# Kernel optimization log

Measured on AMD Instinct MI355X. Metric: run time of the kernel, lower is better.

## Reference

```python
import jax, jax.numpy as jnp
import numpy as np

LMAX = 8                         # lmax-1 used by s2/so3 irreps
DIMS = [2 * l + 1 for l in range(LMAX + 1)]
S2_OFF = np.cumsum([0] + DIMS).tolist()            # offsets into 81-dim s2 irreps
SO3_OFF = np.cumsum([0] + [d * d for d in DIMS]).tolist()  # offsets into 969-dim so3 irreps
S2_DIM = S2_OFF[-1]              # 81
SO3_DIM = SO3_OFF[-1]            # 969
F_IN = 81                        # multiplicity into S2Conv
F_SO3 = 300
C = 768                          # encoder feature channels
KS = 7                           # encoder feature map / kernel size
B = 8
G_S2 = 48                        # s2 healpix grid rec_level=1
G_ACT = 4096                     # SO3Activation grid points (stand-in for res=20 grid)
G_SO3 = 36864                    # so3 healpix grid rec_level=3


def setup_inputs() -> dict:
    key = jax.random.key(0)
    ks = jax.random.split(key, 7)
    return {
        "x": jax.random.normal(ks[0], (B, C, KS, KS), jnp.float32),
        "F": jax.random.normal(ks[1], (F_IN, S2_DIM * C, KS, KS), jnp.float32) * 0.02,
        "w_s2": jax.random.normal(ks[2], (F_IN, F_SO3, G_S2), jnp.float32) * 0.1,
        "Y": jax.random.normal(ks[3], (G_S2, S2_DIM), jnp.float32),
        "w_so3": jax.random.normal(ks[4], (F_SO3, 1, G_SO3), jnp.float32) * 0.1,
        "D": jax.random.normal(ks[5], (G_SO3, SO3_DIM), jnp.float32),
        "D_act": jax.random.normal(ks[6], (G_ACT, SO3_DIM), jnp.float32),
    }


def _forward(x, F, w_s2, Y, w_so3, D, D_act):
    b = x.shape[0]
    # ---- Induction layer: split expanded R2Conv filter into 768-channel chunks,
    # stack, contract with feature map. g_split: (n=81, c_out=81, C, 7, 7)
    g = jnp.swapaxes(F.reshape(F_IN, S2_DIM, C, KS, KS), 0, 1)
    y = jnp.einsum('ijkhw,akhw->aji', g, x)          # (B, 81, 81): (batch, f_in, s2 irreps)

    # ---- S2Conv: expand kernel into irrep space, per-l block linear (s2 -> so3 irreps)
    psi = jnp.einsum('ni,xyn->xyi', Y, w_s2) / np.sqrt(G_S2)  # (81, 300, 81)
    outs = []
    for l, d in enumerate(DIMS):
        o = S2_OFF[l]
        xl = y[:, :, o:o + d]                        # (B, f_in, 2l+1)
        wl = psi[:, :, o:o + d]                      # (f_in, f_out, mul_out=2l+1)
        ol = jnp.einsum('bfm,fgu->bgum', xl, wl) / np.sqrt(F_IN)
        outs.append(ol.reshape(b, F_SO3, d * d))
    z = jnp.concatenate(outs, axis=-1)               # (B, 300, 969)

    # ---- SO3Activation: to grid, relu, back to irreps
    s = jnp.einsum('bfi,gi->bfg', z, D_act)
    z = jnp.einsum('bfg,gi->bfi', jax.nn.relu(s), D_act) / G_ACT

    # ---- SO3Conv: expand kernel via Wigner-D buffer, per-l block linear (so3 -> so3)
    psi2 = jnp.einsum('ni,xyn->xyi', D, w_so3) / np.sqrt(G_SO3)  # (300, 1, 969)
    outs = []
    for l, d in enumerate(DIMS):
        o = SO3_OFF[l]
        xl = z[:, :, o:o + d * d].reshape(b, F_SO3, d, d)   # (B, f, u, m)
        wl = psi2[:, :, o:o + d * d].reshape(F_SO3, 1, d, d)  # (f, g, v, u)
        ol = jnp.einsum('bfum,fgvu->bgvm', xl, wl) / np.sqrt(F_SO3 * d)
        outs.append(ol.reshape(b, 1, d * d))
    return jnp.concatenate(outs, axis=-1)            # (B, 1, 969)


def reference(x, F, w_s2, Y, w_so3, D, D_act):
    return _forward(x, F, w_s2, Y, w_so3, D, D_act)
```

## Files before the change

kernel.cpp:

```cpp
#include <hip/hip_runtime.h>
#include <hip/hip_bf16.h>
#include <math.h>

#define THREADS 256

constexpr int B_    = 8;
constexpr int C_    = 768;
constexpr int KS_   = 7;
constexpr int F_IN  = 81;
constexpr int F_SO3 = 300;
constexpr int S2_DIM  = 81;
constexpr int SO3_DIM = 969;
constexpr int G_S2  = 48;
constexpr int G_ACT = 4096;
constexpr int G_SO3 = 36864;
constexpr int CKK   = C_ * KS_ * KS_;
constexpr int CKK4  = CKK / 4;
constexpr int NPAIR = F_IN * S2_DIM;

constexpr int D2_SPLIT = 4;
constexpr int E1_SPLIT = 32;
constexpr int F_SPLIT  = 5;

__constant__ int d_S2_OFF[10]  = {0, 1, 4, 9, 16, 25, 36, 49, 64, 81};
__constant__ int d_SO3_OFF[10] = {0, 1, 10, 35, 84, 165, 286, 455, 680, 969};

using short8 = __attribute__((ext_vector_type(8))) short;
using f32x4  = __attribute__((ext_vector_type(4))) float;

#define GL16(gp, lp)                                                        \
  __builtin_amdgcn_global_load_lds(                                         \
      (const __attribute__((address_space(1))) void*)(gp),                  \
      (__attribute__((address_space(3))) void*)(lp), 16, 0, 0)

constexpr size_t AL(size_t x) { return (x + 1023) & ~(size_t)1023; }
constexpr size_t O_Y     = 0;
constexpr size_t O_PSI   = O_Y     + AL((size_t)8 * NPAIR * 4);
constexpr size_t O_ZBF   = O_PSI   + AL((size_t)F_IN * F_SO3 * 81 * 4);
constexpr size_t O_DACT  = O_ZBF   + AL((size_t)2432 * 1024 * 2);
constexpr size_t O_DACTT = O_DACT  + AL((size_t)4096 * 1024 * 2);
constexpr size_t O_WSO3  = O_DACTT + AL((size_t)1024 * 4096 * 2);
constexpr size_t O_DT    = O_WSO3  + AL((size_t)384 * 36864 * 2);
constexpr size_t O_SBF   = O_DT    + AL((size_t)1024 * 36864 * 2);
constexpr size_t O_D2P   = O_SBF   + AL((size_t)2432 * 4096 * 2);
constexpr size_t O_Z2P   = O_D2P   + AL((size_t)D2_SPLIT * 2432 * 1024 * 4);
constexpr size_t O_E1P   = O_Z2P   + AL((size_t)2432 * 1024 * 4);
constexpr size_t O_PSI2  = O_E1P   + AL((size_t)E1_SPLIT * 384 * 1024 * 4);
constexpr size_t O_SFP   = O_PSI2  + AL((size_t)F_SO3 * SO3_DIM * 4);
constexpr size_t FAST_NEED = O_SFP + AL((size_t)F_SPLIT * 8 * SO3_DIM * 4);

constexpr size_t WS_Y    = 0;
constexpr size_t WS_PSI  = 52488;
constexpr size_t WS_Z    = 2020788;
constexpr size_t WS_S    = 4346388;
constexpr size_t WS_Z2   = 14176788;
constexpr size_t WS_P2P  = 16502388;
constexpr size_t WS_PSI2 = 18827988;

__global__ __launch_bounds__(THREADS) void k_stage_a3(
    const float* __restrict__ Fm, const float* __restrict__ x, float* __restrict__ y) {
  const int p0  = blockIdx.x * 3;
  const int tid = threadIdx.x;
  const float4* __restrict__ F4 = (const float4*)Fm;
  const float4* __restrict__ x4 = (const float4*)x;

  float acc[3][8];
#pragma unroll
  for (int p = 0; p < 3; ++p)
#pragma unroll
    for (int b = 0; b < 8; ++b) acc[p][b] = 0.f;

  for (int i = tid; i < CKK4; i += THREADS) {
    float4 xv[8];
#pragma unroll
    for (int b = 0; b < 8; ++b) xv[b] = x4[b * CKK4 + i];
#pragma unroll
    for (int p = 0; p < 3; ++p) {
      float4 fv = F4[(size_t)(p0 + p) * CKK4 + i];
#pragma unroll
      for (int b = 0; b < 8; ++b)
        acc[p][b] += fv.x * xv[b].x + fv.y * xv[b].y + fv.z * xv[b].z + fv.w * xv[b].w;
    }
  }

  __shared__ float red[4][24];
  const int lane = tid & 63, wid = tid >> 6;
#pragma unroll
  for (int p = 0; p < 3; ++p) {
#pragma unroll
    for (int b = 0; b < 8; ++b) {
      float v = acc[p][b];
      v += __shfl_down(v, 32);
      v += __shfl_down(v, 16);
      v += __shfl_down(v, 8);
      v += __shfl_down(v, 4);
      v += __shfl_down(v, 2);
      v += __shfl_down(v, 1);
      if (lane == 0) red[wid][p * 8 + b] = v;
    }
  }
  __syncthreads();
  if (tid < 24) {
    float v = red[0][tid] + red[1][tid] + red[2][tid] + red[3][tid];
    int p = tid / 8, b = tid % 8;
    y[(size_t)b * NPAIR + p0 + p] = v;
  }
}

__global__ __launch_bounds__(THREADS) void k_psi(
    const float* __restrict__ w_s2, const float* __restrict__ Y, float* __restrict__ psi) {
  int idx = blockIdx.x * THREADS + threadIdx.x;
  if (idx >= F_IN * F_SO3 * S2_DIM) return;
  int s  = idx % S2_DIM;
  int fg = idx / S2_DIM;
  const float* w = w_s2 + (size_t)fg * G_S2;
  float acc = 0.f;
#pragma unroll 8
  for (int n = 0; n < G_S2; ++n) acc += w[n] * Y[n * S2_DIM + s];
  psi[idx] = acc * 0.14433756729740643f;
}

__global__ __launch_bounds__(THREADS) void k_stage_c_bf(
    const float* __restrict__ y, const float* __restrict__ psi, __hip_bfloat16* __restrict__ z) {
  const int b = blockIdx.x / F_SO3;
  const int g = blockIdx.x % F_SO3;
  __shared__ float ybl[NPAIR];
  __shared__ float psl[NPAIR];
  const int tid = threadIdx.x;
  for (int t = tid; t < NPAIR; t += THREADS) {
    ybl[t] = y[(size_t)b * NPAIR + t];
    int f = t / S2_DIM, s = t % S2_DIM;
    psl[t] = psi[((size_t)f * F_SO3 + g) * S2_DIM + s];
  }
  __syncthreads();
  for (int i = tid; i < 1024; i += THREADS) {
    float acc = 0.f;
    if (i < SO3_DIM) {
      int l = 0;
      while (i >= d_SO3_OFF[l + 1]) ++l;
      int d  = 2 * l + 1;
      int r  = i - d_SO3_OFF[l];
      int u  = r / d, m = r - u * d;
      int so = d_S2_OFF[l];
#pragma unroll 9
      for (int f = 0; f < F_IN; ++f)
        acc += ybl[f * S2_DIM + so + m] * psl[f * S2_DIM + so + u];
      acc *= (1.0f / 9.0f);
    }
    z[((size_t)b * F_SO3 + g) * 1024 + i] = __float2bfloat16(acc);
  }
}

__global__ __launch_bounds__(THREADS) void k_stage_c(
    const float* __restrict__ y, const float* __restrict__ psi, float* __restrict__ z) {
  const int b = blockIdx.x / F_SO3;
  const int g = blockIdx.x % F_SO3;
  __shared__ float ybl[NPAIR];
  __shared__ float psl[NPAIR];
  const int tid = threadIdx.x;
  for (int t = tid; t < NPAIR; t += THREADS) {
    ybl[t] = y[(size_t)b * NPAIR + t];
    int f = t / S2_DIM, s = t % S2_DIM;
    psl[t] = psi[((size_t)f * F_SO3 + g) * S2_DIM + s];
  }
  __syncthreads();
  for (int i = tid; i < SO3_DIM; i += THREADS) {
    int l = 0;
    while (i >= d_SO3_OFF[l + 1]) ++l;
    int d  = 2 * l + 1;
    int r  = i - d_SO3_OFF[l];
    int u  = r / d, m = r - u * d;
    int so = d_S2_OFF[l];
    float acc = 0.f;
#pragma unroll 9
    for (int f = 0; f < F_IN; ++f)
      acc += ybl[f * S2_DIM + so + m] * psl[f * S2_DIM + so + u];
    z[((size_t)b * F_SO3 + g) * SO3_DIM + i] = acc * (1.0f / 9.0f);
  }
}

__global__ __launch_bounds__(THREADS) void k_cvt_pad(
    const float* __restrict__ src, __hip_bfloat16* __restrict__ dst,
    int R, int Cs, int Cp, int Rp) {
  size_t idx = (size_t)blockIdx.x * THREADS + threadIdx.x;
  size_t total = (size_t)Rp * Cp;
  if (idx >= total) return;
  int r = (int)(idx / Cp), c = (int)(idx % Cp);
  float v = (r < R && c < Cs) ? src[(size_t)r * Cs + c] : 0.f;
  dst[idx] = __float2bfloat16(v);
}

__global__ __launch_bounds__(THREADS) void k_transpose_cvt(
    const float* __restrict__ src, __hip_bfloat16* __restrict__ dst,
    int R, int Cs, size_t dstStride) {
  __shared__ float tile[32][33];
  const int c0 = blockIdx.x * 32, r0 = blockIdx.y * 32;
  const int tx = threadIdx.x & 31, ty = threadIdx.x >> 5;
#pragma unroll
  for (int i = 0; i < 32; i += 8) {
    int r = r0 + ty + i, c = c0 + tx;
    tile[ty + i][tx] = (r < R && c < Cs) ? src[(size_t)r * Cs + c] : 0.f;
  }
  __syncthreads();
#pragma unroll
  for (int i = 0; i < 32; i += 8) {
    int c = c0 + ty + i, r = r0 + tx;
    if (c < Cs && r < R) dst[(size_t)c * dstStride + r] = __float2bfloat16(tile[tx][ty + i]);
  }
}

template <int EPI>
__global__ __launch_bounds__(THREADS) void k_mfma_nt(
    const __hip_bfloat16* __restrict__ A, const __hip_bfloat16* __restrict__ B,
    void* __restrict__ Cout, int K, int kSpan, int Ncols, float scale, size_t splitStride) {
  __shared__ __align__(16) char smem[32768];
  char* As = smem;
  char* Bs = smem + 16384;

  const int gx = gridDim.x, gy = gridDim.y;
  unsigned nwg = (unsigned)gx * gy * gridDim.z;
  unsigned lin = ((unsigned)blockIdx.z * gy + blockIdx.y) * gx + blockIdx.x;
  if ((nwg & 7u) == 0u) {
    unsigned q = nwg >> 3;
    lin = (lin & 7u) * q + (lin >> 3);
  }
  const int bxi = (int)(lin % (unsigned)gx);
  const unsigned t1 = lin / (unsigned)gx;
  const int byi = (int)(t1 % (unsigned)gy);
  const int bzi = (int)(t1 / (unsigned)gy);

  const int t    = threadIdx.x;
  const int lane = t & 63;
  const int wave = t >> 6;
  const int wr   = wave >> 1, wc = wave & 1;
  const int bm = byi * 128, bn = bxi * 128;
  const int kBegin = bzi * kSpan;
  const int kEnd   = kBegin + kSpan;

  const char* pA[4];
  const char* pB[4];
  int ldsOff[4];
#pragma unroll
  for (int i = 0; i < 4; ++i) {
    int L   = i * 4096 + t * 16;
    int row = L >> 7;
    int kb  = (L & 127) ^ ((row & 7) << 4);
    pA[i] = (const char*)A + ((size_t)(bm + row) * K) * 2 + kb;
    pB[i] = (const char*)B + ((size_t)(bn + row) * K) * 2 + kb;
    ldsOff[i] = L;
  }

  f32x4 acc[4][4] = {};

  for (int k0 = kBegin; k0 < kEnd; k0 += 64) {
    size_t koff = (size_t)k0 * 2;
#pragma unroll
    for (int i = 0; i < 4; ++i) {
      GL16(pA[i] + koff, As + ldsOff[i]);
      GL16(pB[i] + koff, Bs + ldsOff[i]);
    }
    __syncthreads();
#pragma unroll
    for (int kk = 0; kk < 2; ++kk) {
      const int klin = kk * 64 + ((lane >> 4) << 4);
      short8 af[4], bfr[4];
#pragma unroll
      for (int m = 0; m < 4; ++m) {
        int ra = (wr << 6) + (m << 4) + (lane & 15);
        af[m] = *(const short8*)(As + ra * 128 + (klin ^ ((ra & 7) << 4)));
        int rb = (wc << 6) + (m << 4) + (lane & 15);
        bfr[m] = *(const short8*)(Bs + rb * 128 + (klin ^ ((rb & 7) << 4)));
      }
#pragma unroll
      for (int m = 0; m < 4; ++m)
#pragma unroll
        for (int n = 0; n < 4; ++n)
          acc[m][n] = __builtin_amdgcn_mfma_f32_16x16x32_bf16(af[m], bfr[n], acc[m][n], 0, 0, 0);
    }
    __syncthreads();
  }

  const int rbase = bm + (wr << 6) + ((lane >> 4) << 2);
  const int cbase = bn + (wc << 6) + (lane & 15);
  if (EPI == 0) {
    float* C = (float*)Cout + (size_t)bzi * splitStride;
#pragma unroll
    for (int m = 0; m < 4; ++m)
#pragma unroll
      for (int n = 0; n < 4; ++n)
#pragma unroll
        for (int r = 0; r < 4; ++r)
          C[(size_t)(rbase + m * 16 + r) * Ncols + (cbase + n * 16)] = acc[m][n][r] * scale;
  } else {
    __hip_bfloat16* C = (__hip_bfloat16*)Cout;
#pragma unroll
    for (int m = 0; m < 4; ++m)
#pragma unroll
      for (int n = 0; n < 4; ++n)
#pragma unroll
        for (int r = 0; r < 4; ++r)
          C[(size_t)(rbase + m * 16 + r) * Ncols + (cbase + n * 16)] =
              __float2bfloat16(fmaxf(acc[m][n][r], 0.f));
  }
}

__global__ __launch_bounds__(THREADS) void k_reduce_split(
    const float* __restrict__ parts, float* __restrict__ dst, int R, int C,
    size_t rowStride, size_t splitStride, size_t dstStride, int nSplit, float scale) {
  int idx = blockIdx.x * THREADS + threadIdx.x;
  if (idx >= R * C) return;
  int r = idx / C, c = idx % C;
  float a = 0.f;
  for (int s = 0; s < nSplit; ++s) a += parts[(size_t)s * splitStride + (size_t)r * rowStride + c];
  dst[(size_t)r * dstStride + c] = a * scale;
}

__global__ __launch_bounds__(THREADS) void k_stage_f_part(
    const float* __restrict__ z2, const float* __restrict__ psi2, float* __restrict__ partial,
    int zStride) {
  const int b  = blockIdx.x / 9;
  const int l  = blockIdx.x % 9;
  const int sp = blockIdx.y;
  const int d = 2 * l + 1, d2 = d * d;
  const int off = d_SO3_OFF[l];
  __shared__ float zb[10][289];
  __shared__ float pb[10][289];
  const int tid = threadIdx.x;
  float acc[2] = {0.f, 0.f};
  const int fBeg = sp * (F_SO3 / F_SPLIT), fEnd = fBeg + F_SO3 / F_SPLIT;
  for (int fc = fBeg; fc < fEnd; fc += 10) {
    for (int t = tid; t < 10 * d2; t += THREADS) {
      int fl = t / d2, q = t - fl * d2;
      int f  = fc + fl;
      zb[fl][q] = z2[((size_t)b * F_SO3 + f) * zStride + off + q];
      pb[fl][q] = psi2[(size_t)f * SO3_DIM + off + q];
    }
    __syncthreads();
#pragma unroll 2
    for (int io = 0; io < 2; ++io) {
      int i = tid + io * THREADS;
      if (i < d2) {
        int v = i / d, m = i - v * d;
        float a = acc[io];
#pragma unroll
        for (int fl = 0; fl < 10; ++fl) {
          float s_ = 0.f;
          for (int u = 0; u < d; ++u)
            s_ += zb[fl][u * d + m] * pb[fl][v * d + u];
          a += s_;
        }
        acc[io] = a;
      }
    }
    __syncthreads();
  }
  for (int io = 0; io < 2; ++io) {
    int i = tid + io * THREADS;
    if (i < d2) partial[((size_t)sp * 8 + b) * SO3_DIM + off + i] = acc[io];
  }
}

__global__ __launch_bounds__(THREADS) void k_stage_f_red(
    const float* __restrict__ partial, float* __restrict__ out) {
  int idx = blockIdx.x * THREADS + threadIdx.x;
  if (idx >= 8 * SO3_DIM) return;
  int b = idx / SO3_DIM, i = idx % SO3_DIM;
  int l = 0;
  while (i >= d_SO3_OFF[l + 1]) ++l;
  float a = 0.f;
#pragma unroll
  for (int sp = 0; sp < F_SPLIT; ++sp)
    a += partial[((size_t)sp * 8 + b) * SO3_DIM + i];
  out[(size_t)b * SO3_DIM + i] = a * rsqrtf(300.0f * (float)(2 * l + 1));
}

__global__ __launch_bounds__(THREADS) void k_gemm_nt_relu(
    const float* __restrict__ A, const float* __restrict__ Bm, float* __restrict__ Cm,
    int M, int N, int K) {
  __shared__ float As[16][68];
  __shared__ float Bs[16][68];
  const int bm = blockIdx.y * 64, bn = blockIdx.x * 64;
  const int t  = threadIdx.x;
  const int lk = t & 15, lm = t >> 4;
  const int tn = t & 15, tm = t >> 4;
  float acc[4][4] = {};
  for (int k0 = 0; k0 < K; k0 += 16) {
    int gk = k0 + lk;
#pragma unroll
    for (int j = 0; j < 4; ++j) {
      int m  = lm + 16 * j;
      int gm = bm + m;
      As[lk][m] = (gm < M && gk < K) ? A[(size_t)gm * K + gk] : 0.f;
      int gn = bn + m;
      Bs[lk][m] = (gn < N && gk < K) ? Bm[(size_t)gn * K + gk] : 0.f;
    }
    __syncthreads();
#pragma unroll
    for (int k = 0; k < 16; ++k) {
      float4 av = *(const float4*)&As[k][tm * 4];
      float4 bv = *(const float4*)&Bs[k][tn * 4];
      float a[4] = {av.x, av.y, av.z, av.w};
      float bb[4] = {bv.x, bv.y, bv.z, bv.w};
#pragma unroll
      for (int i2 = 0; i2 < 4; ++i2)
#pragma unroll
        for (int j2 = 0; j2 < 4; ++j2)
          acc[i2][j2] += a[i2] * bb[j2];
    }
    __syncthreads();
  }
#pragma unroll
  for (int i2 = 0; i2 < 4; ++i2) {
    int gm = bm + tm * 4 + i2;
    if (gm >= M) continue;
#pragma unroll
    for (int j2 = 0; j2 < 4; ++j2) {
      int gn = bn + tn * 4 + j2;
      if (gn < N) Cm[(size_t)gm * N + gn] = fmaxf(acc[i2][j2], 0.f);
    }
  }
}

__global__ __launch_bounds__(THREADS) void k_gemm_nn(
    const float* __restrict__ A, const float* __restrict__ Bm, float* __restrict__ Cm,
    int M, int N, int K, int kSpan, float scale, size_t cStride) {
  __shared__ float As[16][68];
  __shared__ float Bs[16][68];
  const int bm = blockIdx.y * 64, bn = blockIdx.x * 64;
  const int t   = threadIdx.x;
  const int lk  = t & 15, lm = t >> 4;
  const int ln  = t & 63, lkq = t >> 6;
  const int tn  = t & 15, tm = t >> 4;
  const int kBegin = blockIdx.z * kSpan;
  const int kEnd   = kBegin + kSpan;
  float* C = Cm + (size_t)blockIdx.z * cStride;
  float acc[4][4] = {};
  for (int k0 = kBegin; k0 < kEnd; k0 += 16) {
    {
      int gk = k0 + lk;
#pragma unroll
      for (int j = 0; j < 4; ++j) {
        int m = lm + 16 * j, gm = bm + m;
        As[lk][m] = (gm < M) ? A[(size_t)gm * K + gk] : 0.f;
      }
    }
    {
      int gn = bn + ln;
#pragma unroll
      for (int j = 0; j < 4; ++j) {
        int k = lkq + 4 * j;
        Bs[k][ln] = (gn < N) ? Bm[(size_t)(k0 + k) * N + gn] : 0.f;
      }
    }
    __syncthreads();
#pragma unroll
    for (int k = 0; k < 16; ++k) {
      float4 av = *(const float4*)&As[k][tm * 4];
      float4 bv = *(const float4*)&Bs[k][tn * 4];
      float a[4] = {av.x, av.y, av.z, av.w};
      float bb[4] = {bv.x, bv.y, bv.z, bv.w};
#pragma unroll
      for (int i2 = 0; i2 < 4; ++i2)
#pragma unroll
        for (int j2 = 0; j2 < 4; ++j2)
          acc[i2][j2] += a[i2] * bb[j2];
    }
    __syncthreads();
  }
#pragma unroll
  for (int i2 = 0; i2 < 4; ++i2) {
    int gm = bm + tm * 4 + i2;
    if (gm >= M) continue;
#pragma unroll
    for (int j2 = 0; j2 < 4; ++j2) {
      int gn = bn + tn * 4 + j2;
      if (gn < N) C[(size_t)gm * N + gn] = acc[i2][j2] * scale;
    }
  }
}

__global__ __launch_bounds__(THREADS) void k_reduce_psi2(
    const float* __restrict__ parts, float* __restrict__ psi2) {
  int idx = blockIdx.x * THREADS + threadIdx.x;
  if (idx >= F_SO3 * SO3_DIM) return;
  float acc = 0.f;
#pragma unroll
  for (int s = 0; s < 8; ++s) acc += parts[(size_t)s * (F_SO3 * SO3_DIM) + idx];
  psi2[idx] = acc * (1.0f / 192.0f);
}

__global__ __launch_bounds__(THREADS) void k_stage_f(
    const float* __restrict__ z2, const float* __restrict__ psi2, float* __restrict__ out,
    int zStride) {
  const int b = blockIdx.x / 9;
  const int l = blockIdx.x % 9;
  const int d = 2 * l + 1, d2 = d * d;
  const int off = d_SO3_OFF[l];
  __shared__ float zb[10][289];
  __shared__ float pb[10][289];
  const int tid = threadIdx.x;
  float acc[2] = {0.f, 0.f};
  const float scale = rsqrtf(300.0f * (float)d);
  for (int fc = 0; fc < F_SO3; fc += 10) {
    for (int t = tid; t < 10 * d2; t += THREADS) {
      int fl = t / d2, q = t - fl * d2;
      int f  = fc + fl;
      zb[fl][q] = z2[((size_t)b * F_SO3 + f) * zStride + off + q];
      pb[fl][q] = psi2[(size_t)f * SO3_DIM + off + q];
    }
    __syncthreads();
#pragma unroll 2
    for (int io = 0; io < 2; ++io) {
      int i = tid + io * THREADS;
      if (i < d2) {
        int v = i / d, m = i - v * d;
        float a = acc[io];
#pragma unroll
        for (int fl = 0; fl < 10; ++fl) {
          float s_ = 0.f;
          for (int u = 0; u < d; ++u)
            s_ += zb[fl][u * d + m] * pb[fl][v * d + u];
          a += s_;
        }
        acc[io] = a;
      }
    }
    __syncthreads();
  }
  for (int io = 0; io < 2; ++io) {
    int i = tid + io * THREADS;
    if (i < d2) out[(size_t)b * SO3_DIM + off + i] = acc[io] * scale;
  }
}

extern "C" void kernel_launch(void* const* d_in, const int* in_sizes, int n_in,
                              void* d_out, int out_size, void* d_ws, size_t ws_size,
                              hipStream_t stream) {
  const float* x     = (const float*)d_in[0];
  const float* Fm    = (const float*)d_in[1];
  const float* w_s2  = (const float*)d_in[2];
  const float* Y     = (const float*)d_in[3];
  const float* w_so3 = (const float*)d_in[4];
  const float* D     = (const float*)d_in[5];
  const float* D_act = (const float*)d_in[6];
  float* out = (float*)d_out;

  if (ws_size >= FAST_NEED) {
    char* p = (char*)d_ws;
    float*          y       = (float*)(p + O_Y);
    float*          psi     = (float*)(p + O_PSI);
    __hip_bfloat16* z_bf    = (__hip_bfloat16*)(p + O_ZBF);
    __hip_bfloat16* Dact_bf = (__hip_bfloat16*)(p + O_DACT);
    __hip_bfloat16* DactT_bf= (__hip_bfloat16*)(p + O_DACTT);
    __hip_bfloat16* wso3_bf = (__hip_bfloat16*)(p + O_WSO3);
    __hip_bfloat16* DT_bf   = (__hip_bfloat16*)(p + O_DT);
    __hip_bfloat16* s_bf    = (__hip_bfloat16*)(p + O_SBF);
    float*          d2p     = (float*)(p + O_D2P);
    float*          z2p     = (float*)(p + O_Z2P);
    float*          e1p     = (float*)(p + O_E1P);
    float*          psi2    = (float*)(p + O_PSI2);
    float*          sfp     = (float*)(p + O_SFP);

    k_cvt_pad<<<(4096 * 1024 + THREADS - 1) / THREADS, THREADS, 0, stream>>>(
        D_act, Dact_bf, G_ACT, SO3_DIM, 1024, 4096);
    k_transpose_cvt<<<dim3(31, 128), THREADS, 0, stream>>>(D_act, DactT_bf, G_ACT, SO3_DIM, 4096);
    k_cvt_pad<<<(384 * 36864 + THREADS - 1) / THREADS, THREADS, 0, stream>>>(
        w_so3, wso3_bf, F_SO3, G_SO3, G_SO3, 384);
    k_transpose_cvt<<<dim3(31, 1152), THREADS, 0, stream>>>(D, DT_bf, G_SO3, SO3_DIM, 36864);

    k_stage_a3<<<NPAIR / 3, THREADS, 0, stream>>>(Fm, x, y);
    k_psi<<<(F_IN * F_SO3 * S2_DIM + THREADS - 1) / THREADS, THREADS, 0, stream>>>(w_s2, Y, psi);
    k_stage_c_bf<<<B_ * F_SO3, THREADS, 0, stream>>>(y, psi, z_bf);

    k_mfma_nt<1><<<dim3(32, 19, 1), THREADS, 0, stream>>>(
        z_bf, Dact_bf, s_bf, 1024, 1024, 4096, 1.f, 0);
    k_mfma_nt<0><<<dim3(8, 19, D2_SPLIT), THREADS, 0, stream>>>(
        s_bf, DactT_bf, d2p, 4096, 4096 / D2_SPLIT, 1024, 1.f, (size_t)2432 * 1024);
    k_reduce_split<<<(2400 * 969 + THREADS - 1) / THREADS, THREADS, 0, stream>>>(
        d2p, z2p, 2400, 969, 1024, (size_t)2432 * 1024, 1024, D2_SPLIT, 1.0f / G_ACT);
    k_mfma_nt<0><<<dim3(8, 3, E1_SPLIT), THREADS, 0, stream>>>(
        wso3_bf, DT_bf, e1p, G_SO3, G_SO3 / E1_SPLIT, 1024, 1.f, (size_t)384 * 1024);
    k_reduce_split<<<(300 * 969 + THREADS - 1) / THREADS, THREADS, 0, stream>>>(
        e1p, psi2, 300, 969, 1024, (size_t)384 * 1024, 969, E1_SPLIT, 1.0f / 192.0f);

    k_stage_f_part<<<dim3(B_ * 9, F_SPLIT), THREADS, 0, stream>>>(z2p, psi2, sfp, 1024);
    k_stage_f_red<<<(8 * SO3_DIM + THREADS - 1) / THREADS, THREADS, 0, stream>>>(sfp, out);
  } else {
    float* ws  = (float*)d_ws;
    float* y    = ws + WS_Y;
    float* psi  = ws + WS_PSI;
    float* z    = ws + WS_Z;
    float* s    = ws + WS_S;
    float* z2   = ws + WS_Z2;
    float* p2p  = ws + WS_P2P;
    float* psi2 = ws + WS_PSI2;

    k_stage_a3<<<NPAIR / 3, THREADS, 0, stream>>>(Fm, x, y);
    k_psi<<<(F_IN * F_SO3 * S2_DIM + THREADS - 1) / THREADS, THREADS, 0, stream>>>(w_s2, Y, psi);
    k_stage_c<<<B_ * F_SO3, THREADS, 0, stream>>>(y, psi, z);
    k_gemm_nt_relu<<<dim3(G_ACT / 64, (B_ * F_SO3 + 63) / 64), THREADS, 0, stream>>>(
        z, D_act, s, B_ * F_SO3, G_ACT, SO3_DIM);
    k_gemm_nn<<<dim3((SO3_DIM + 63) / 64, (B_ * F_SO3 + 63) / 64, 1), THREADS, 0, stream>>>(
        s, D_act, z2, B_ * F_SO3, SO3_DIM, G_ACT, G_ACT, 1.0f / G_ACT, 0);
    k_gemm_nn<<<dim3((SO3_DIM + 63) / 64, (F_SO3 + 63) / 64, 8), THREADS, 0, stream>>>(
        w_so3, D, p2p, F_SO3, SO3_DIM, G_SO3, G_SO3 / 8, 1.0f, (size_t)F_SO3 * SO3_DIM);
    k_reduce_psi2<<<(F_SO3 * SO3_DIM + THREADS - 1) / THREADS, THREADS, 0, stream>>>(p2p, psi2);
    k_stage_f<<<B_ * 9, THREADS, 0, stream>>>(z2, psi2, out, SO3_DIM);
  }
}
```

Before: 642.8 us.

## Merge preprocessing and independent GEMMs into combined launches, fold split reduction

The four bf16 conversion/transpose kernels and the psi kernel are merged into one large block-indexed kernel. The E1 GEMM and the first activation GEMM run together in one dual launch, and the D2 GEMM shares a launch with the E1 split-K reduction. The D2 split reduction is folded into the stage-F loader, which removes the z2p buffer. E1 split-K drops from 32 to 16, a constexpr lookup table replaces the per-element l search, and F loads become nontemporal. This cuts launch count and gives the scheduler independent work to overlap, at the cost of mixing heterogeneous blocks in one grid and uneven block lifetimes.

After: 611.0 us. 5.0% less time.

```diff
diff --git a/kernel.cpp b/kernel.cpp
--- a/kernel.cpp
+++ b/kernel.cpp
@@ -19,14 +19,34 @@
 constexpr int NPAIR = F_IN * S2_DIM;
 
 constexpr int D2_SPLIT = 4;
-constexpr int E1_SPLIT = 32;
+constexpr int E1_SPLIT = 16;
 constexpr int F_SPLIT  = 5;
 
 __constant__ int d_S2_OFF[10]  = {0, 1, 4, 9, 16, 25, 36, 49, 64, 81};
 __constant__ int d_SO3_OFF[10] = {0, 1, 10, 35, 84, 165, 286, 455, 680, 969};
 
+struct CEnt { unsigned char u, m, so, l; };
+struct CLut { CEnt v[992]; };
+constexpr CLut make_clut() {
+  CLut t{};
+  int S2O[10]  = {0, 1, 4, 9, 16, 25, 36, 49, 64, 81};
+  int SO3O[10] = {0, 1, 10, 35, 84, 165, 286, 455, 680, 969};
+  for (int i = 0; i < 969; ++i) {
+    int l = 0;
+    while (i >= SO3O[l + 1]) ++l;
+    int d = 2 * l + 1, r = i - SO3O[l];
+    t.v[i].u  = (unsigned char)(r / d);
+    t.v[i].m  = (unsigned char)(r % d);
+    t.v[i].so = (unsigned char)S2O[l];
+    t.v[i].l  = (unsigned char)l;
+  }
+  return t;
+}
+__constant__ CLut g_clut = make_clut();
+
 using short8 = __attribute__((ext_vector_type(8))) short;
 using f32x4  = __attribute__((ext_vector_type(4))) float;
+using f4v    = __attribute__((ext_vector_type(4))) float;
 
 #define GL16(gp, lp)                                                        \
   __builtin_amdgcn_global_load_lds(                                         \
@@ -43,8 +63,7 @@
 constexpr size_t O_DT    = O_WSO3  + AL((size_t)384 * 36864 * 2);
 constexpr size_t O_SBF   = O_DT    + AL((size_t)1024 * 36864 * 2);
 constexpr size_t O_D2P   = O_SBF   + AL((size_t)2432 * 4096 * 2);
-constexpr size_t O_Z2P   = O_D2P   + AL((size_t)D2_SPLIT * 2432 * 1024 * 4);
-constexpr size_t O_E1P   = O_Z2P   + AL((size_t)2432 * 1024 * 4);
+constexpr size_t O_E1P   = O_D2P   + AL((size_t)D2_SPLIT * 2432 * 1024 * 4);
 constexpr size_t O_PSI2  = O_E1P   + AL((size_t)E1_SPLIT * 384 * 1024 * 4);
 constexpr size_t O_SFP   = O_PSI2  + AL((size_t)F_SO3 * SO3_DIM * 4);
 constexpr size_t FAST_NEED = O_SFP + AL((size_t)F_SPLIT * 8 * SO3_DIM * 4);
@@ -61,8 +80,8 @@
     const float* __restrict__ Fm, const float* __restrict__ x, float* __restrict__ y) {
   const int p0  = blockIdx.x * 3;
   const int tid = threadIdx.x;
-  const float4* __restrict__ F4 = (const float4*)Fm;
-  const float4* __restrict__ x4 = (const float4*)x;
+  const f4v* __restrict__ F4 = (const f4v*)Fm;
+  const f4v* __restrict__ x4 = (const f4v*)x;
 
   float acc[3][8];
 #pragma unroll
@@ -71,15 +90,15 @@
     for (int b = 0; b < 8; ++b) acc[p][b] = 0.f;
 
   for (int i = tid; i < CKK4; i += THREADS) {
-    float4 xv[8];
+    f4v xv[8];
 #pragma unroll
     for (int b = 0; b < 8; ++b) xv[b] = x4[b * CKK4 + i];
 #pragma unroll
     for (int p = 0; p < 3; ++p) {
-      float4 fv = F4[(size_t)(p0 + p) * CKK4 + i];
+      f4v fv = __builtin_nontemporal_load(&F4[(size_t)(p0 + p) * CKK4 + i]);
 #pragma unroll
       for (int b = 0; b < 8; ++b)
-        acc[p][b] += fv.x * xv[b].x + fv.y * xv[b].y + fv.z * xv[b].z + fv.w * xv[b].w;
+        acc[p][b] += fv[0] * xv[b][0] + fv[1] * xv[b][1] + fv[2] * xv[b][2] + fv[3] * xv[b][3];
     }
   }
 
@@ -107,9 +126,38 @@
   }
 }
 
-__global__ __launch_bounds__(THREADS) void k_psi(
-    const float* __restrict__ w_s2, const float* __restrict__ Y, float* __restrict__ psi) {
-  int idx = blockIdx.x * THREADS + threadIdx.x;
+__device__ __forceinline__ void cvt_body(const float* __restrict__ src,
+                                         __hip_bfloat16* __restrict__ dst,
+                                         int R, int Cs, int Cp, int blk) {
+  size_t idx = (size_t)blk * THREADS + threadIdx.x;
+  int r = (int)(idx / (unsigned)Cp), c = (int)(idx % (unsigned)Cp);
+  float v = (r < R && c < Cs) ? src[(size_t)r * Cs + c] : 0.f;
+  dst[idx] = __float2bfloat16(v);
+}
+
+__device__ __forceinline__ void tr_body(const float* __restrict__ src,
+                                        __hip_bfloat16* __restrict__ dst,
+                                        int R, int Cs, size_t dstStride, int bx, int by) {
+  __shared__ float tile[32][33];
+  const int c0 = bx * 32, r0 = by * 32;
+  const int tx = threadIdx.x & 31, ty = threadIdx.x >> 5;
+#pragma unroll
+  for (int i = 0; i < 32; i += 8) {
+    int r = r0 + ty + i, c = c0 + tx;
+    tile[ty + i][tx] = (r < R && c < Cs) ? src[(size_t)r * Cs + c] : 0.f;
+  }
+  __syncthreads();
+#pragma unroll
+  for (int i = 0; i < 32; i += 8) {
+    int c = c0 + ty + i, r = r0 + tx;
+    if (c < Cs && r < R) dst[(size_t)c * dstStride + r] = __float2bfloat16(tile[tx][ty + i]);
+  }
+}
+
+__device__ __forceinline__ void psi_body(const float* __restrict__ w_s2,
+                                         const float* __restrict__ Y,
+                                         float* __restrict__ psi, int blk) {
+  int idx = blk * THREADS + threadIdx.x;
   if (idx >= F_IN * F_SO3 * S2_DIM) return;
   int s  = idx % S2_DIM;
   int fg = idx / S2_DIM;
@@ -118,6 +166,31 @@
 #pragma unroll 8
   for (int n = 0; n < G_S2; ++n) acc += w[n] * Y[n * S2_DIM + s];
   psi[idx] = acc * 0.14433756729740643f;
+}
+
+constexpr int UB1 = 16384;
+constexpr int UB2 = 3968;
+constexpr int UB3 = 55296;
+constexpr int UB4 = 35712;
+constexpr int UB5 = 7689;
+constexpr int UB_TOT = UB1 + UB2 + UB3 + UB4 + UB5;
+
+__global__ __launch_bounds__(THREADS) void k_uber(
+    const float* __restrict__ D_act, __hip_bfloat16* __restrict__ Dact_bf,
+    __hip_bfloat16* __restrict__ DactT_bf,
+    const float* __restrict__ w_so3, __hip_bfloat16* __restrict__ wso3_bf,
+    const float* __restrict__ D, __hip_bfloat16* __restrict__ DT_bf,
+    const float* __restrict__ w_s2, const float* __restrict__ Y, float* __restrict__ psi) {
+  int b = blockIdx.x;
+  if (b < UB1) { cvt_body(D_act, Dact_bf, G_ACT, SO3_DIM, 1024, b); return; }
+  b -= UB1;
+  if (b < UB2) { tr_body(D_act, DactT_bf, G_ACT, SO3_DIM, 4096, b % 31, b / 31); return; }
+  b -= UB2;
+  if (b < UB3) { cvt_body(w_so3, wso3_bf, F_SO3, G_SO3, G_SO3, b); return; }
+  b -= UB3;
+  if (b < UB4) { tr_body(D, DT_bf, G_SO3, SO3_DIM, 36864, b % 31, b / 31); return; }
+  b -= UB4;
+  psi_body(w_s2, Y, psi, b);
 }
 
 __global__ __launch_bounds__(THREADS) void k_stage_c_bf(
@@ -136,19 +209,198 @@
   for (int i = tid; i < 1024; i += THREADS) {
     float acc = 0.f;
     if (i < SO3_DIM) {
-      int l = 0;
-      while (i >= d_SO3_OFF[l + 1]) ++l;
-      int d  = 2 * l + 1;
-      int r  = i - d_SO3_OFF[l];
-      int u  = r / d, m = r - u * d;
-      int so = d_S2_OFF[l];
+      CEnt e = g_clut.v[i];
+      int im = e.so + e.m, iu = e.so + e.u;
 #pragma unroll 9
       for (int f = 0; f < F_IN; ++f)
-        acc += ybl[f * S2_DIM + so + m] * psl[f * S2_DIM + so + u];
+        acc += ybl[f * S2_DIM + im] * psl[f * S2_DIM + iu];
       acc *= (1.0f / 9.0f);
     }
     z[((size_t)b * F_SO3 + g) * 1024 + i] = __float2bfloat16(acc);
   }
+}
+
+struct GemmDesc {
+  const __hip_bfloat16* A;
+  const __hip_bfloat16* B;
+  void* C;
+  int K, kSpan, Ncols;
+  float scale;
+  size_t splitStride;
+  int gx, gy, gz, epi;
+};
+
+__device__ __forceinline__ void mfma_nt_body(const GemmDesc g, unsigned lin) {
+  __shared__ __align__(16) char smem[32768];
+  char* As = smem;
+  char* Bs = smem + 16384;
+
+  unsigned nwg = (unsigned)(g.gx * g.gy * g.gz);
+  if ((nwg & 7u) == 0u) {
+    unsigned q = nwg >> 3;
+    lin = (lin & 7u) * q + (lin >> 3);
+  }
+  const int bxi = (int)(lin % (unsigned)g.gx);
+  const unsigned t1 = lin / (unsigned)g.gx;
+  const int byi = (int)(t1 % (unsigned)g.gy);
+  const int bzi = (int)(t1 / (unsigned)g.gy);
+
+  const int t    = threadIdx.x;
+  const int lane = t & 63;
+  const int wave = t >> 6;
+  const int wr   = wave >> 1, wc = wave & 1;
+  const int bm = byi * 128, bn = bxi * 128;
+  const int kBegin = bzi * g.kSpan;
+  const int kEnd   = kBegin + g.kSpan;
+
+  const char* pA[4];
+  const char* pB[4];
+  int ldsOff[4];
+#pragma unroll
+  for (int i = 0; i < 4; ++i) {
+    int L   = i * 4096 + t * 16;
+    int row = L >> 7;
+    int kb  = (L & 127) ^ ((row & 7) << 4);
+    pA[i] = (const char*)g.A + ((size_t)(bm + row) * g.K) * 2 + kb;
+    pB[i] = (const char*)g.B + ((size_t)(bn + row) * g.K) * 2 + kb;
+    ldsOff[i] = L;
+  }
+
+  f32x4 acc[4][4] = {};
+
+  for (int k0 = kBegin; k0 < kEnd; k0 += 64) {
+    size_t koff = (size_t)k0 * 2;
+#pragma unroll
+    for (int i = 0; i < 4; ++i) {
+      GL16(pA[i] + koff, As + ldsOff[i]);
+      GL16(pB[i] + koff, Bs + ldsOff[i]);
+    }
+    __syncthreads();
+#pragma unroll
+    for (int kk = 0; kk < 2; ++kk) {
+      const int klin = kk * 64 + ((lane >> 4) << 4);
+      short8 af[4], bfr[4];
+#pragma unroll
+      for (int m = 0; m < 4; ++m) {
+        int ra = (wr << 6) + (m << 4) + (lane & 15);
+        af[m] = *(const short8*)(As + ra * 128 + (klin ^ ((ra & 7) << 4)));
+        int rb = (wc << 6) + (m << 4) + (lane & 15);
+        bfr[m] = *(const short8*)(Bs + rb * 128 + (klin ^ ((rb & 7) << 4)));
+      }
+#pragma unroll
+      for (int m = 0; m < 4; ++m)
+#pragma unroll
+        for (int n = 0; n < 4; ++n)
+          acc[m][n] = __builtin_amdgcn_mfma_f32_16x16x32_bf16(af[m], bfr[n], acc[m][n], 0, 0, 0);
+    }
+    __syncthreads();
+  }
+
+  const int rbase = bm + (wr << 6) + ((lane >> 4) << 2);
+  const int cbase = bn + (wc << 6) + (lane & 15);
+  if (g.epi == 0) {
+    float* C = (float*)g.C + (size_t)bzi * g.splitStride;
+#pragma unroll
+    for (int m = 0; m < 4; ++m)
+#pragma unroll
+      for (int n = 0; n < 4; ++n)
+#pragma unroll
+        for (int r = 0; r < 4; ++r)
+          C[(size_t)(rbase + m * 16 + r) * g.Ncols + (cbase + n * 16)] = acc[m][n][r] * g.scale;
+  } else {
+    __hip_bfloat16* C = (__hip_bfloat16*)g.C;
+#pragma unroll
+    for (int m = 0; m < 4; ++m)
+#pragma unroll
+      for (int n = 0; n < 4; ++n)
+#pragma unroll
+        for (int r = 0; r < 4; ++r)
+          C[(size_t)(rbase + m * 16 + r) * g.Ncols + (cbase + n * 16)] =
+              __float2bfloat16(fmaxf(acc[m][n][r], 0.f));
+  }
+}
+
+__global__ __launch_bounds__(THREADS) void k_mfma_dual(GemmDesc g0, GemmDesc g1, int n0) {
+  if ((int)blockIdx.x < n0) mfma_nt_body(g0, blockIdx.x);
+  else                      mfma_nt_body(g1, blockIdx.x - n0);
+}
+
+__global__ __launch_bounds__(THREADS) void k_mfma_reduce(
+    GemmDesc g, int n0,
+    const float* __restrict__ parts, float* __restrict__ dst, int R, int C,
+    size_t rowStride, size_t splitStride, size_t dstStride, int nSplit, float scale) {
+  if ((int)blockIdx.x < n0) { mfma_nt_body(g, blockIdx.x); return; }
+  int idx = (int)(blockIdx.x - n0) * THREADS + threadIdx.x;
+  if (idx >= R * C) return;
+  int r = idx / C, c = idx % C;
+  float a = 0.f;
+  for (int s = 0; s < nSplit; ++s) a += parts[(size_t)s * splitStride + (size_t)r * rowStride + c];
+  dst[(size_t)r * dstStride + c] = a * scale;
+}
+
+__global__ __launch_bounds__(THREADS) void k_stage_f_part(
+    const float* __restrict__ d2p, const float* __restrict__ psi2, float* __restrict__ partial) {
+  const int b  = blockIdx.x / 9;
+  const int l  = blockIdx.x % 9;
+  const int sp = blockIdx.y;
+  const int d = 2 * l + 1, d2 = d * d;
+  const int off = d_SO3_OFF[l];
+  constexpr size_t SS = (size_t)2432 * 1024;
+  __shared__ float zb[10][289];
+  __shared__ float pb[10][289];
+  const int tid = threadIdx.x;
+  float acc[2] = {0.f, 0.f};
+  const int fBeg = sp * (F_SO3 / F_SPLIT), fEnd = fBeg + F_SO3 / F_SPLIT;
+  for (int fc = fBeg; fc < fEnd; fc += 10) {
+    for (int t = tid; t < 10 * d2; t += THREADS) {
+      int fl = t / d2, q = t - fl * d2;
+      int f  = fc + fl;
+      size_t zi = ((size_t)b * F_SO3 + f) * 1024 + off + q;
+      float zv = d2p[zi] + d2p[zi + SS] + d2p[zi + 2 * SS] + d2p[zi + 3 * SS];
+      zb[fl][q] = zv * (1.0f / G_ACT);
+      pb[fl][q] = psi2[(size_t)f * SO3_DIM + off + q];
+    }
+    __syncthreads();
+#pragma unroll 2
+    for (int io = 0; io < 2; ++io) {
+      int i = tid + io * THREADS;
+      if (i < d2) {
+        int v = i / d, m = i - v * d;
+        float a = acc[io];
+#pragma unroll
+        for (int fl = 0; fl < 10; ++fl) {
+          float s_ = 0.f;
+          for (int u = 0; u < d; ++u)
+            s_ += zb[fl][u * d + m] * pb[fl][v * d + u];
+          a += s_;
+        }
+        acc[io] = a;
+      }
+    }
+    __syncthreads();
+  }
+  for (int io = 0; io < 2; ++io) {
+    int i = tid + io * THREADS;
+    if (i < d2) partial[((size_t)sp * 8 + b) * SO3_DIM + off + i] = acc[io];
+  }
+}
+
+__global__ __launch_bounds__(THREADS) void k_stage_f_red(
+    const float* __restrict__ partial, float* __restrict__ out) {
+  int idx = blockIdx.x * THREADS + threadIdx.x;
+  if (idx >= 8 * SO3_DIM) return;
+  int b = idx / SO3_DIM, i = idx % SO3_DIM;
+  int l = g_clut.v[i].l;
+  float a = 0.f;
+#pragma unroll
+  for (int sp = 0; sp < F_SPLIT; ++sp)
+    a += partial[((size_t)sp * 8 + b) * SO3_DIM + i];
+  out[(size_t)b * SO3_DIM + i] = a * rsqrtf(300.0f * (float)(2 * l + 1));
+}
+
+__global__ __launch_bounds__(THREADS) void k_psi(
+    const float* __restrict__ w_s2, const float* __restrict__ Y, float* __restrict__ psi) {
+  psi_body(w_s2, Y, psi, blockIdx.x);
 }
 
 __global__ __launch_bounds__(THREADS) void k_stage_c(
@@ -165,213 +417,14 @@
   }
   __syncthreads();
   for (int i = tid; i < SO3_DIM; i += THREADS) {
-    int l = 0;
-    while (i >= d_SO3_OFF[l + 1]) ++l;
-    int d  = 2 * l + 1;
-    int r  = i - d_SO3_OFF[l];
-    int u  = r / d, m = r - u * d;
-    int so = d_S2_OFF[l];
+    CEnt e = g_clut.v[i];
+    int im = e.so + e.m, iu = e.so + e.u;
     float acc = 0.f;
 #pragma unroll 9
     for (int f = 0; f < F_IN; ++f)
-      acc += ybl[f * S2_DIM + so + m] * psl[f * S2_DIM + so + u];
+      acc += ybl[f * S2_DIM + im] * psl[f * S2_DIM + iu];
     z[((size_t)b * F_SO3 + g) * SO3_DIM + i] = acc * (1.0f / 9.0f);
   }
-}
-
-__global__ __launch_bounds__(THREADS) void k_cvt_pad(
-    const float* __restrict__ src, __hip_bfloat16* __restrict__ dst,
-    int R, int Cs, int Cp, int Rp) {
-  size_t idx = (size_t)blockIdx.x * THREADS + threadIdx.x;
-  size_t total = (size_t)Rp * Cp;
-  if (idx >= total) return;
-  int r = (int)(idx / Cp), c = (int)(idx % Cp);
-  float v = (r < R && c < Cs) ? src[(size_t)r * Cs + c] : 0.f;
-  dst[idx] = __float2bfloat16(v);
-}
-
-__global__ __launch_bounds__(THREADS) void k_transpose_cvt(
-    const float* __restrict__ src, __hip_bfloat16* __restrict__ dst,
-    int R, int Cs, size_t dstStride) {
-  __shared__ float tile[32][33];
-  const int c0 = blockIdx.x * 32, r0 = blockIdx.y * 32;
-  const int tx = threadIdx.x & 31, ty = threadIdx.x >> 5;
-#pragma unroll
-  for (int i = 0; i < 32; i += 8) {
-    int r = r0 + ty + i, c = c0 + tx;
-    tile[ty + i][tx] = (r < R && c < Cs) ? src[(size_t)r * Cs + c] : 0.f;
-  }
-  __syncthreads();
-#pragma unroll
-  for (int i = 0; i < 32; i += 8) {
-    int c = c0 + ty + i, r = r0 + tx;
-    if (c < Cs && r < R) dst[(size_t)c * dstStride + r] = __float2bfloat16(tile[tx][ty + i]);
-  }
-}
-
-template <int EPI>
-__global__ __launch_bounds__(THREADS) void k_mfma_nt(
-    const __hip_bfloat16* __restrict__ A, const __hip_bfloat16* __restrict__ B,
-    void* __restrict__ Cout, int K, int kSpan, int Ncols, float scale, size_t splitStride) {
-  __shared__ __align__(16) char smem[32768];
-  char* As = smem;
-  char* Bs = smem + 16384;
-
-  const int gx = gridDim.x, gy = gridDim.y;
-  unsigned nwg = (unsigned)gx * gy * gridDim.z;
-  unsigned lin = ((unsigned)blockIdx.z * gy + blockIdx.y) * gx + blockIdx.x;
-  if ((nwg & 7u) == 0u) {
-    unsigned q = nwg >> 3;
-    lin = (lin & 7u) * q + (lin >> 3);
-  }
-  const int bxi = (int)(lin % (unsigned)gx);
-  const unsigned t1 = lin / (unsigned)gx;
-  const int byi = (int)(t1 % (unsigned)gy);
-  const int bzi = (int)(t1 / (unsigned)gy);
-
-  const int t    = threadIdx.x;
-  const int lane = t & 63;
-  const int wave = t >> 6;
-  const int wr   = wave >> 1, wc = wave & 1;
-  const int bm = byi * 128, bn = bxi * 128;
-  const int kBegin = bzi * kSpan;
-  const int kEnd   = kBegin + kSpan;
-
-  const char* pA[4];
-  const char* pB[4];
-  int ldsOff[4];
-#pragma unroll
-  for (int i = 0; i < 4; ++i) {
-    int L   = i * 4096 + t * 16;
-    int row = L >> 7;
-    int kb  = (L & 127) ^ ((row & 7) << 4);
-    pA[i] = (const char*)A + ((size_t)(bm + row) * K) * 2 + kb;
-    pB[i] = (const char*)B + ((size_t)(bn + row) * K) * 2 + kb;
-    ldsOff[i] = L;
-  }
-
-  f32x4 acc[4][4] = {};
-
-  for (int k0 = kBegin; k0 < kEnd; k0 += 64) {
-    size_t koff = (size_t)k0 * 2;
-#pragma unroll
-    for (int i = 0; i < 4; ++i) {
-      GL16(pA[i] + koff, As + ldsOff[i]);
-      GL16(pB[i] + koff, Bs + ldsOff[i]);
-    }
-    __syncthreads();
-#pragma unroll
-    for (int kk = 0; kk < 2; ++kk) {
-      const int klin = kk * 64 + ((lane >> 4) << 4);
-      short8 af[4], bfr[4];
-#pragma unroll
-      for (int m = 0; m < 4; ++m) {
-        int ra = (wr << 6) + (m << 4) + (lane & 15);
-        af[m] = *(const short8*)(As + ra * 128 + (klin ^ ((ra & 7) << 4)));
-        int rb = (wc << 6) + (m << 4) + (lane & 15);
-        bfr[m] = *(const short8*)(Bs + rb * 128 + (klin ^ ((rb & 7) << 4)));
-      }
-#pragma unroll
-      for (int m = 0; m < 4; ++m)
-#pragma unroll
-        for (int n = 0; n < 4; ++n)
-          acc[m][n] = __builtin_amdgcn_mfma_f32_16x16x32_bf16(af[m], bfr[n], acc[m][n], 0, 0, 0);
-    }
-    __syncthreads();
-  }
-
-  const int rbase = bm + (wr << 6) + ((lane >> 4) << 2);
-  const int cbase = bn + (wc << 6) + (lane & 15);
-  if (EPI == 0) {
-    float* C = (float*)Cout + (size_t)bzi * splitStride;
-#pragma unroll
-    for (int m = 0; m < 4; ++m)
-#pragma unroll
-      for (int n = 0; n < 4; ++n)
-#pragma unroll
-        for (int r = 0; r < 4; ++r)
-          C[(size_t)(rbase + m * 16 + r) * Ncols + (cbase + n * 16)] = acc[m][n][r] * scale;
-  } else {
-    __hip_bfloat16* C = (__hip_bfloat16*)Cout;
-#pragma unroll
-    for (int m = 0; m < 4; ++m)
-#pragma unroll
-      for (int n = 0; n < 4; ++n)
-#pragma unroll
-        for (int r = 0; r < 4; ++r)
-          C[(size_t)(rbase + m * 16 + r) * Ncols + (cbase + n * 16)] =
-              __float2bfloat16(fmaxf(acc[m][n][r], 0.f));
-  }
-}
-
-__global__ __launch_bounds__(THREADS) void k_reduce_split(
-    const float* __restrict__ parts, float* __restrict__ dst, int R, int C,
-    size_t rowStride, size_t splitStride, size_t dstStride, int nSplit, float scale) {
-  int idx = blockIdx.x * THREADS + threadIdx.x;
-  if (idx >= R * C) return;
-  int r = idx / C, c = idx % C;
-  float a = 0.f;
-  for (int s = 0; s < nSplit; ++s) a += parts[(size_t)s * splitStride + (size_t)r * rowStride + c];
-  dst[(size_t)r * dstStride + c] = a * scale;
-}
-
-__global__ __launch_bounds__(THREADS) void k_stage_f_part(
-    const float* __restrict__ z2, const float* __restrict__ psi2, float* __restrict__ partial,
-    int zStride) {
-  const int b  = blockIdx.x / 9;
-  const int l  = blockIdx.x % 9;
-  const int sp = blockIdx.y;
-  const int d = 2 * l + 1, d2 = d * d;
-  const int off = d_SO3_OFF[l];
-  __shared__ float zb[10][289];
-  __shared__ float pb[10][289];
-  const int tid = threadIdx.x;
-  float acc[2] = {0.f, 0.f};
-  const int fBeg = sp * (F_SO3 / F_SPLIT), fEnd = fBeg + F_SO3 / F_SPLIT;
-  for (int fc = fBeg; fc < fEnd; fc += 10) {
-    for (int t = tid; t < 10 * d2; t += THREADS) {
-      int fl = t / d2, q = t - fl * d2;
-      int f  = fc + fl;
-      zb[fl][q] = z2[((size_t)b * F_SO3 + f) * zStride + off + q];
-      pb[fl][q] = psi2[(size_t)f * SO3_DIM + off + q];
-    }
-    __syncthreads();
-#pragma unroll 2
-    for (int io = 0; io < 2; ++io) {
-      int i = tid + io * THREADS;
-      if (i < d2) {
-        int v = i / d, m = i - v * d;
-        float a = acc[io];
-#pragma unroll
-        for (int fl = 0; fl < 10; ++fl) {
-          float s_ = 0.f;
-          for (int u = 0; u < d; ++u)
-            s_ += zb[fl][u * d + m] * pb[fl][v * d + u];
-          a += s_;
-        }
-        acc[io] = a;
-      }
-    }
-    __syncthreads();
-  }
-  for (int io = 0; io < 2; ++io) {
-    int i = tid + io * THREADS;
-    if (i < d2) partial[((size_t)sp * 8 + b) * SO3_DIM + off + i] = acc[io];
-  }
-}
-
-__global__ __launch_bounds__(THREADS) void k_stage_f_red(
-    const float* __restrict__ partial, float* __restrict__ out) {
-  int idx = blockIdx.x * THREADS + threadIdx.x;
-  if (idx >= 8 * SO3_DIM) return;
-  int b = idx / SO3_DIM, i = idx % SO3_DIM;
-  int l = 0;
-  while (i >= d_SO3_OFF[l + 1]) ++l;
-  float a = 0.f;
-#pragma unroll
-  for (int sp = 0; sp < F_SPLIT; ++sp)
-    a += partial[((size_t)sp * 8 + b) * SO3_DIM + i];
-  out[(size_t)b * SO3_DIM + i] = a * rsqrtf(300.0f * (float)(2 * l + 1));
 }
 
 __global__ __launch_bounds__(THREADS) void k_gemm_nt_relu(
@@ -556,34 +609,31 @@
     __hip_bfloat16* DT_bf   = (__hip_bfloat16*)(p + O_DT);
     __hip_bfloat16* s_bf    = (__hip_bfloat16*)(p + O_SBF);
     float*          d2p     = (float*)(p + O_D2P);
-    float*          z2p     = (float*)(p + O_Z2P);
     float*          e1p     = (float*)(p + O_E1P);
     float*          psi2    = (float*)(p + O_PSI2);
     float*          sfp     = (float*)(p + O_SFP);
 
-    k_cvt_pad<<<(4096 * 1024 + THREADS - 1) / THREADS, THREADS, 0, stream>>>(
-        D_act, Dact_bf, G_ACT, SO3_DIM, 1024, 4096);
-    k_transpose_cvt<<<dim3(31, 128), THREADS, 0, stream>>>(D_act, DactT_bf, G_ACT, SO3_DIM, 4096);
-    k_cvt_pad<<<(384 * 36864 + THREADS - 1) / THREADS, THREADS, 0, stream>>>(
-        w_so3, wso3_bf, F_SO3, G_SO3, G_SO3, 384);
-    k_transpose_cvt<<<dim3(31, 1152), THREADS, 0, stream>>>(D, DT_bf, G_SO3, SO3_DIM, 36864);
-
     k_stage_a3<<<NPAIR / 3, THREADS, 0, stream>>>(Fm, x, y);
-    k_psi<<<(F_IN * F_SO3 * S2_DIM + THREADS - 1) / THREADS, THREADS, 0, stream>>>(w_s2, Y, psi);
+    k_uber<<<UB_TOT, THREADS, 0, stream>>>(
+        D_act, Dact_bf, DactT_bf, w_so3, wso3_bf, D, DT_bf, w_s2, Y, psi);
     k_stage_c_bf<<<B_ * F_SO3, THREADS, 0, stream>>>(y, psi, z_bf);
 
-    k_mfma_nt<1><<<dim3(32, 19, 1), THREADS, 0, stream>>>(
-        z_bf, Dact_bf, s_bf, 1024, 1024, 4096, 1.f, 0);
-    k_mfma_nt<0><<<dim3(8, 19, D2_SPLIT), THREADS, 0, stream>>>(
-        s_bf, DactT_bf, d2p, 4096, 4096 / D2_SPLIT, 1024, 1.f, (size_t)2432 * 1024);
-    k_reduce_split<<<(2400 * 969 + THREADS - 1) / THREADS, THREADS, 0, stream>>>(
-        d2p, z2p, 2400, 969, 1024, (size_t)2432 * 1024, 1024, D2_SPLIT, 1.0f / G_ACT);
-    k_mfma_nt<0><<<dim3(8, 3, E1_SPLIT), THREADS, 0, stream>>>(
-        wso3_bf, DT_bf, e1p, G_SO3, G_SO3 / E1_SPLIT, 1024, 1.f, (size_t)384 * 1024);
-    k_reduce_split<<<(300 * 969 + THREADS - 1) / THREADS, THREADS, 0, stream>>>(
-        e1p, psi2, 300, 969, 1024, (size_t)384 * 1024, 969, E1_SPLIT, 1.0f / 192.0f);
-
-    k_stage_f_part<<<dim3(B_ * 9, F_SPLIT), THREADS, 0, stream>>>(z2p, psi2, sfp, 1024);
+    GemmDesc e1{wso3_bf, DT_bf, e1p, G_SO3, G_SO3 / E1_SPLIT, 1024, 1.f,
+                (size_t)384 * 1024, 8, 3, E1_SPLIT, 0};
+    GemmDesc d1{z_bf, Dact_bf, s_bf, 1024, 1024, 4096, 1.f, 0, 32, 19, 1, 1};
+    int nE1 = 8 * 3 * E1_SPLIT;
+    int nD1 = 32 * 19;
+    k_mfma_dual<<<nE1 + nD1, THREADS, 0, stream>>>(e1, d1, nE1);
+
+    GemmDesc d2{s_bf, DactT_bf, d2p, 4096, 4096 / D2_SPLIT, 1024, 1.f,
+                (size_t)2432 * 1024, 8, 19, D2_SPLIT, 0};
+    int nD2 = 8 * 19 * D2_SPLIT;
+    int nE1r = (F_SO3 * SO3_DIM + THREADS - 1) / THREADS;
+    k_mfma_reduce<<<nD2 + nE1r, THREADS, 0, stream>>>(
+        d2, nD2, e1p, psi2, F_SO3, SO3_DIM, 1024, (size_t)384 * 1024, SO3_DIM,
+        E1_SPLIT, 1.0f / 192.0f);
+
+    k_stage_f_part<<<dim3(B_ * 9, F_SPLIT), THREADS, 0, stream>>>(d2p, psi2, sfp);
     k_stage_f_red<<<(8 * SO3_DIM + THREADS - 1) / THREADS, THREADS, 0, stream>>>(sfp, out);
   } else {
     float* ws  = (float*)d_ws;
```
